# Kernel optimization log

Measured on AMD Instinct MI355X. Metric: run time of the kernel, lower is better.

The kernel has to match this reference:

```python
import jax, jax.numpy as jnp
import numpy as np

ALPHA = 0.2          # LeakyReLU negative slope
NEG = -9e15          # mask fill value, as in pyGAT GraphAttentionLayer
N, NIN, NHID, NOUT = 4096, 64, 32, 64
NHEADS, D_INT = 8, 32
H_INT = max(1, int(NHEADS * 0.25))   # 2 intent heads
H_SP = NHEADS - H_INT                # 6 spatial heads


def setup_inputs() -> dict:
    key = jax.random.key(0)
    ks = jax.random.split(key, 10)
    x = jax.random.normal(ks[0], (N, NIN), dtype=jnp.float32)
    adj = (jax.random.uniform(ks[1], (N, N)) < 0.01).astype(jnp.float32)
    adj = jnp.clip(adj + jnp.eye(N, dtype=jnp.float32), 0.0, 1.0)
    intent_embeds = jax.random.normal(ks[2], (N, D_INT), dtype=jnp.float32)
    # learned params (xavier-ish scale)
    def xav(k, shape):
        fan = shape[-2] if len(shape) > 1 else shape[-1]
        return jax.random.normal(k, shape, dtype=jnp.float32) / np.sqrt(fan)
    W_sp = xav(ks[3], (H_SP, NIN, NHID))       # spatial head projections
    a_sp = xav(ks[4], (H_SP, 2 * NHID))        # spatial attention vectors
    W_int = xav(ks[5], (H_INT, NIN, NHID))     # intent head projections
    a_int = xav(ks[6], (H_INT, 2 * D_INT))     # intent attention vectors (over intent embeds)
    W_out = xav(ks[7], (NHID * NHEADS, NOUT))  # output GAT layer
    a_out = xav(ks[8], (2 * NOUT,))
    return {"x": x, "adj": adj, "intent_embeds": intent_embeds,
            "W_sp": W_sp, "a_sp": a_sp, "W_int": W_int, "a_int": a_int,
            "W_out": W_out, "a_out": a_out}


def _masked_attend(e, mask, Wh):
    # e: [H,N,N] raw scores, mask: [1,N,N] bool, Wh: [H,N,F]
    att = jax.nn.softmax(jnp.where(mask, e, NEG), axis=-1)
    return jnp.einsum('hij,hjf->hif', att, Wh)


def reference(x, adj, intent_embeds, W_sp, a_sp, W_int, a_int, W_out, a_out):
    mask = (adj > 0)[None]                                   # [1,N,N]
    # ---- spatial heads (standard GAT, batched over heads) ----
    Wh_s = jnp.einsum('nf,hfo->hno', x, W_sp)                # [Hs,N,nhid]
    f1 = jnp.einsum('hno,ho->hn', Wh_s, a_sp[:, :NHID])
    f2 = jnp.einsum('hno,ho->hn', Wh_s, a_sp[:, NHID:])
    e_s = jax.nn.leaky_relu(f1[:, :, None] + f2[:, None, :], ALPHA)
    h_s = jax.nn.elu(_masked_attend(e_s, mask, Wh_s))        # concat=True -> elu
    # ---- intent heads: scores from intent embeddings, values from Wh ----
    Wh_i = jnp.einsum('nf,hfo->hno', x, W_int)               # [Hi,N,nhid]
    g1 = jnp.einsum('nd,hd->hn', intent_embeds, a_int[:, :D_INT])
    g2 = jnp.einsum('nd,hd->hn', intent_embeds, a_int[:, D_INT:])
    e_i = jax.nn.leaky_relu(g1[:, :, None] + g2[:, None, :], ALPHA)
    h_i = jax.nn.elu(_masked_attend(e_i, mask, Wh_i))        # [Hi,N,nhid]
    # ---- concat heads along feature dim: [N, nheads*nhid] ----
    h = jnp.concatenate([h_s, h_i], axis=0).transpose(1, 0, 2).reshape(N, -1)
    # ---- output attention layer (concat=False: no elu) ----
    Who = h @ W_out                                          # [N,nout]
    o1 = Who @ a_out[:NOUT]
    o2 = Who @ a_out[NOUT:]
    e_o = jax.nn.leaky_relu(o1[:, None] + o2[None, :], ALPHA)
    att_o = jax.nn.softmax(jnp.where(mask[0], e_o, NEG), axis=-1)
    out = att_o @ Who
    return jnp.tanh(out)
```

## Files before the change

### kernel.cpp

```cpp
#include <hip/hip_runtime.h>

#define N      4096
#define NIN    64
#define NHID   32
#define NOUT   64
#define NHEADS 8
#define H_SP   6
#define D_INT  32
#define MAXDEG 128
#define NPB    4
#define ALPHA  0.2f

__global__ __launch_bounds__(256) void k_fused1(
    const float* __restrict__ x, const float* __restrict__ ie,
    const float4* __restrict__ adj4,
    const float* __restrict__ Wsp, const float* __restrict__ asp,
    const float* __restrict__ Wint, const float* __restrict__ aint,
    float* __restrict__ Wh_t, float* __restrict__ src, float* __restrict__ dst_t,
    int* __restrict__ col, int* __restrict__ deg)
{
    const int nb   = blockIdx.x * NPB;
    const int tid  = threadIdx.x;
    const int wv   = tid >> 6, lane = tid & 63;
    const int h    = tid >> 5, f    = tid & 31;

    __shared__ float xs[NPB][NIN];
    __shared__ float ies[NPB][D_INT];

    xs[tid >> 6][tid & 63] = x[nb * NIN + tid];
    if (tid < NPB * D_INT) ies[tid >> 5][tid & 31] = ie[nb * D_INT + tid];
    __syncthreads();

    const float* W = (h < H_SP) ? (Wsp + h * NIN * NHID)
                                : (Wint + (h - H_SP) * NIN * NHID);
    float acc[NPB] = {0.f, 0.f, 0.f, 0.f};
#pragma unroll
    for (int c = 0; c < NIN; ++c) {
        const float wval = W[c * NHID + f];
#pragma unroll
        for (int m = 0; m < NPB; ++m) acc[m] += xs[m][c] * wval;
    }
#pragma unroll
    for (int m = 0; m < NPB; ++m)
        Wh_t[(size_t)(nb + m) * 256 + tid] = acc[m];

    const float a1v = (h < H_SP) ? asp[h * 64 + f]      : aint[(h - H_SP) * 64 + f];
    const float a2v = (h < H_SP) ? asp[h * 64 + 32 + f] : aint[(h - H_SP) * 64 + 32 + f];
#pragma unroll
    for (int m = 0; m < NPB; ++m) {
        const float b = (h < H_SP) ? acc[m] : ies[m][f];
        float s1 = b * a1v, s2 = b * a2v;
#pragma unroll
        for (int mm = 16; mm >= 1; mm >>= 1) {
            s1 += __shfl_xor(s1, mm);
            s2 += __shfl_xor(s2, mm);
        }
        if (f == 0) { src[h * N + nb + m] = s1; dst_t[(nb + m) * 8 + h] = s2; }
    }

    const int r = nb + wv;
    const float4* row = adj4 + (size_t)r * (N / 4);
    int cnt = 0;
#pragma unroll 4
    for (int t = 0; t < 16; ++t) {
        float4 v = row[t * 64 + lane];
        unsigned nib = (v.x > 0.f ? 1u : 0u) | (v.y > 0.f ? 2u : 0u)
                     | (v.z > 0.f ? 4u : 0u) | (v.w > 0.f ? 8u : 0u);
        int c = __popc(nib);
        int scan = c;
#pragma unroll
        for (int m = 1; m <= 32; m <<= 1) {
            int o = __shfl_up(scan, m);
            if (lane >= m) scan += o;
        }
        int pos = cnt + scan - c;
        int idx0 = (t * 64 + lane) * 4;
        if (nib) {
            if (nib & 1u) { if (pos < MAXDEG) col[r * MAXDEG + pos] = idx0;     ++pos; }
            if (nib & 2u) { if (pos < MAXDEG) col[r * MAXDEG + pos] = idx0 + 1; ++pos; }
            if (nib & 4u) { if (pos < MAXDEG) col[r * MAXDEG + pos] = idx0 + 2; ++pos; }
            if (nib & 8u) { if (pos < MAXDEG) col[r * MAXDEG + pos] = idx0 + 3; ++pos; }
        }
        cnt += __shfl(scan, 63);
    }
    if (lane == 0) deg[r] = (cnt < MAXDEG) ? cnt : MAXDEG;
}

__global__ __launch_bounds__(256) void k_attn1who(
    const int* __restrict__ col, const int* __restrict__ deg,
    const float* __restrict__ Wh_t, const float* __restrict__ src,
    const float* __restrict__ dst_t, const float* __restrict__ Wout,
    const float* __restrict__ aout,
    float* __restrict__ Who, float* __restrict__ o1, float* __restrict__ o2)
{
    const int r   = blockIdx.x;
    const int tid = threadIdx.x;
    const int h   = tid >> 5, lane = tid & 31;

    __shared__ int   cs[MAXDEG];
    __shared__ float w[NHEADS][MAXDEG];
    __shared__ float hs[NHEADS * NHID];
    __shared__ float part[4][NOUT];

    const int d  = deg[r];
    const int d8 = (d + 7) & ~7;
    for (int k = tid; k < MAXDEG; k += 256)
        cs[k] = (k < d) ? col[r * MAXDEG + k] : 0;
    __syncthreads();

    const float sr = src[h * N + r];
    float ev[4];
    float mx = -3.4e38f;
#pragma unroll
    for (int t = 0; t < 4; ++t) {
        int k = lane + t * 32;
        float e = -3.4e38f;
        if (k < d) {
            e = sr + dst_t[cs[k] * 8 + h];
            e = e > 0.f ? e : ALPHA * e;
        }
        ev[t] = e;
        mx = fmaxf(mx, e);
    }
#pragma unroll
    for (int m = 16; m >= 1; m >>= 1) mx = fmaxf(mx, __shfl_xor(mx, m));

    float sum = 0.f;
#pragma unroll
    for (int t = 0; t < 4; ++t) {
        int k = lane + t * 32;
        float p = (k < d) ? __expf(ev[t] - mx) : 0.f;
        ev[t] = p;
        sum += p;
    }
#pragma unroll
    for (int m = 16; m >= 1; m >>= 1) sum += __shfl_xor(sum, m);
    const float inv = 1.f / sum;

#pragma unroll
    for (int t = 0; t < 4; ++t) {
        int k = lane + t * 32;
        w[h][k] = (k < d) ? ev[t] * inv : 0.f;
    }
    __syncthreads();

    float acc0 = 0.f, acc1 = 0.f;
    for (int k = 0; k < d8; k += 8) {
        int4   ja = *(const int4*)  &cs[k];
        int4   jb = *(const int4*)  &cs[k + 4];
        float4 wa = *(const float4*)&w[h][k];
        float4 wb = *(const float4*)&w[h][k + 4];
        float g0 = Wh_t[(size_t)ja.x * 256 + tid];
        float g1 = Wh_t[(size_t)ja.y * 256 + tid];
        float g2 = Wh_t[(size_t)ja.z * 256 + tid];
        float g3 = Wh_t[(size_t)ja.w * 256 + tid];
        float g4 = Wh_t[(size_t)jb.x * 256 + tid];
        float g5 = Wh_t[(size_t)jb.y * 256 + tid];
        float g6 = Wh_t[(size_t)jb.z * 256 + tid];
        float g7 = Wh_t[(size_t)jb.w * 256 + tid];
        acc0 += wa.x * g0 + wa.y * g1 + wa.z * g2 + wa.w * g3;
        acc1 += wb.x * g4 + wb.y * g5 + wb.z * g6 + wb.w * g7;
    }
    float acc = acc0 + acc1;
    acc = acc > 0.f ? acc : __expf(acc) - 1.f;
    hs[tid] = acc;
    __syncthreads();

    const int fo = tid & 63, q = tid >> 6;
    float p = 0.f;
#pragma unroll
    for (int c = q * 64; c < q * 64 + 64; ++c) p += hs[c] * Wout[c * NOUT + fo];
    part[q][fo] = p;
    __syncthreads();

    if (tid < 64) {
        float who = part[0][tid] + part[1][tid] + part[2][tid] + part[3][tid];
        Who[(size_t)r * NOUT + tid] = who;
        float v1 = who * aout[tid];
        float v2 = who * aout[NOUT + tid];
#pragma unroll
        for (int m = 32; m >= 1; m >>= 1) {
            v1 += __shfl_xor(v1, m);
            v2 += __shfl_xor(v2, m);
        }
        if (tid == 0) { o1[r] = v1; o2[r] = v2; }
    }
}

__global__ __launch_bounds__(256) void k_attn2(
    const int* __restrict__ col, const int* __restrict__ deg,
    const float* __restrict__ Who, const float* __restrict__ o1,
    const float* __restrict__ o2, float* __restrict__ out)
{
    const int r   = blockIdx.x;
    const int tid = threadIdx.x;
    const int wv  = tid >> 6, lane = tid & 63;

    __shared__ int   cs[MAXDEG];
    __shared__ float w[MAXDEG];
    __shared__ float part[4][NOUT];
    __shared__ float redm[4], reds[4];

    const int d = deg[r];
    for (int k = tid; k < MAXDEG; k += 256)
        cs[k] = (k < d) ? col[r * MAXDEG + k] : 0;
    __syncthreads();

    const float sr = o1[r];
    float e = -3.4e38f;
    if (tid < d) {
        e = sr + o2[cs[tid]];
        e = e > 0.f ? e : ALPHA * e;
    }
    float mx = e;
#pragma unroll
    for (int m = 32; m >= 1; m >>= 1) mx = fmaxf(mx, __shfl_xor(mx, m));
    if (lane == 0) redm[wv] = mx;
    __syncthreads();
    mx = fmaxf(fmaxf(redm[0], redm[1]), fmaxf(redm[2], redm[3]));

    float p = (tid < d) ? __expf(e - mx) : 0.f;
    float s = p;
#pragma unroll
    for (int m = 32; m >= 1; m >>= 1) s += __shfl_xor(s, m);
    if (lane == 0) reds[wv] = s;
    __syncthreads();
    const float inv = 1.f / (reds[0] + reds[1] + reds[2] + reds[3]);
    if (tid < MAXDEG) w[tid] = p * inv;
    __syncthreads();

    const int kup = (d + 31) & ~31;
    float acc0 = 0.f, acc1 = 0.f;
    for (int k = wv * 8; k < kup; k += 32) {
        int4   ja = *(const int4*)  &cs[k];
        int4   jb = *(const int4*)  &cs[k + 4];
        float4 wa = *(const float4*)&w[k];
        float4 wb = *(const float4*)&w[k + 4];
        acc0 += wa.x * Who[(size_t)ja.x * NOUT + lane];
        acc0 += wa.y * Who[(size_t)ja.y * NOUT + lane];
        acc0 += wa.z * Who[(size_t)ja.z * NOUT + lane];
        acc0 += wa.w * Who[(size_t)ja.w * NOUT + lane];
        acc1 += wb.x * Who[(size_t)jb.x * NOUT + lane];
        acc1 += wb.y * Who[(size_t)jb.y * NOUT + lane];
        acc1 += wb.z * Who[(size_t)jb.z * NOUT + lane];
        acc1 += wb.w * Who[(size_t)jb.w * NOUT + lane];
    }
    part[wv][lane] = acc0 + acc1;
    __syncthreads();

    if (tid < NOUT)
        out[(size_t)r * NOUT + tid] =
            tanhf(part[0][tid] + part[1][tid] + part[2][tid] + part[3][tid]);
}

extern "C" void kernel_launch(void* const* d_in, const int* in_sizes, int n_in,
                              void* d_out, int out_size, void* d_ws, size_t ws_size,
                              hipStream_t stream) {
    const float* x    = (const float*)d_in[0];
    const float* adj  = (const float*)d_in[1];
    const float* ie   = (const float*)d_in[2];
    const float* Wsp  = (const float*)d_in[3];
    const float* asp  = (const float*)d_in[4];
    const float* Wint = (const float*)d_in[5];
    const float* aint = (const float*)d_in[6];
    const float* Wout = (const float*)d_in[7];
    const float* aout = (const float*)d_in[8];
    float* out = (float*)d_out;

    float* ws    = (float*)d_ws;
    float* Wh_t  = ws;
    float* src   = Wh_t + 1048576;
    float* dst_t = src  + 32768;
    float* Who   = dst_t + 32768;
    float* o1    = Who  + 262144;
    float* o2    = o1   + 4096;
    int*   col   = (int*)(o2 + 4096);
    int*   deg   = col + 4096 * MAXDEG;

    k_fused1  <<<N / NPB, 256, 0, stream>>>(x, ie, (const float4*)adj, Wsp, asp,
                                            Wint, aint, Wh_t, src, dst_t, col, deg);
    k_attn1who<<<N,       256, 0, stream>>>(col, deg, Wh_t, src, dst_t, Wout, aout,
                                            Who, o1, o2);
    k_attn2   <<<N,       256, 0, stream>>>(col, deg, Who, o1, o2, out);
}
```

Before: 154.7 us.

## Use ballot compaction, batch rows per block, and wave-per-row output attention

The adjacency compaction replaces shuffle-based prefix scans with per-component ballots and mbcnt to compute write positions. The first attention kernel now handles two rows per block, so each Wout load is shared and launch overhead drops. The output attention kernel maps one wavefront per row and broadcasts neighbor indices and weights with readlane, removing shared memory and block barriers. The x tile is also transposed so the projection reads four rows with one vector LDS load. Gather loops for two rows run to the larger degree, which may waste some work.

```diff
diff --git a/kernel.cpp b/kernel.cpp
--- a/kernel.cpp
+++ b/kernel.cpp
@@ -9,7 +9,13 @@
 #define D_INT  32
 #define MAXDEG 128
 #define NPB    4
+#define NPB2   2
 #define ALPHA  0.2f
+
+__device__ __forceinline__ int mbcnt64(unsigned long long m) {
+    return __builtin_amdgcn_mbcnt_hi((unsigned)(m >> 32),
+           __builtin_amdgcn_mbcnt_lo((unsigned)m, 0u));
+}
 
 __global__ __launch_bounds__(256) void k_fused1(
     const float* __restrict__ x, const float* __restrict__ ie,
@@ -24,10 +30,10 @@
     const int wv   = tid >> 6, lane = tid & 63;
     const int h    = tid >> 5, f    = tid & 31;
 
-    __shared__ float xs[NPB][NIN];
+    __shared__ float xs_t[NIN][NPB];
     __shared__ float ies[NPB][D_INT];
 
-    xs[tid >> 6][tid & 63] = x[nb * NIN + tid];
+    xs_t[tid & 63][tid >> 6] = x[nb * NIN + tid];
     if (tid < NPB * D_INT) ies[tid >> 5][tid & 31] = ie[nb * D_INT + tid];
     __syncthreads();
 
@@ -37,8 +43,9 @@
 #pragma unroll
     for (int c = 0; c < NIN; ++c) {
         const float wval = W[c * NHID + f];
-#pragma unroll
-        for (int m = 0; m < NPB; ++m) acc[m] += xs[m][c] * wval;
+        const float4 xv  = *(const float4*)&xs_t[c][0];
+        acc[0] += xv.x * wval; acc[1] += xv.y * wval;
+        acc[2] += xv.z * wval; acc[3] += xv.w * wval;
     }
 #pragma unroll
     for (int m = 0; m < NPB; ++m)
@@ -64,24 +71,22 @@
 #pragma unroll 4
     for (int t = 0; t < 16; ++t) {
         float4 v = row[t * 64 + lane];
-        unsigned nib = (v.x > 0.f ? 1u : 0u) | (v.y > 0.f ? 2u : 0u)
-                     | (v.z > 0.f ? 4u : 0u) | (v.w > 0.f ? 8u : 0u);
-        int c = __popc(nib);
-        int scan = c;
-#pragma unroll
-        for (int m = 1; m <= 32; m <<= 1) {
-            int o = __shfl_up(scan, m);
-            if (lane >= m) scan += o;
-        }
-        int pos = cnt + scan - c;
-        int idx0 = (t * 64 + lane) * 4;
-        if (nib) {
-            if (nib & 1u) { if (pos < MAXDEG) col[r * MAXDEG + pos] = idx0;     ++pos; }
-            if (nib & 2u) { if (pos < MAXDEG) col[r * MAXDEG + pos] = idx0 + 1; ++pos; }
-            if (nib & 4u) { if (pos < MAXDEG) col[r * MAXDEG + pos] = idx0 + 2; ++pos; }
-            if (nib & 8u) { if (pos < MAXDEG) col[r * MAXDEG + pos] = idx0 + 3; ++pos; }
-        }
-        cnt += __shfl(scan, 63);
+        unsigned long long bx = __ballot(v.x > 0.f);
+        unsigned long long by = __ballot(v.y > 0.f);
+        unsigned long long bz = __ballot(v.z > 0.f);
+        unsigned long long bw = __ballot(v.w > 0.f);
+        const int tx = __popcll(bx), ty = __popcll(by);
+        const int tz = __popcll(bz), tw = __popcll(bw);
+        const int idx0 = (t * 64 + lane) * 4;
+        const int px = cnt + mbcnt64(bx);
+        const int py = cnt + tx + mbcnt64(by);
+        const int pz = cnt + tx + ty + mbcnt64(bz);
+        const int pw = cnt + tx + ty + tz + mbcnt64(bw);
+        if (v.x > 0.f && px < MAXDEG) col[r * MAXDEG + px] = idx0;
+        if (v.y > 0.f && py < MAXDEG) col[r * MAXDEG + py] = idx0 + 1;
+        if (v.z > 0.f && pz < MAXDEG) col[r * MAXDEG + pz] = idx0 + 2;
+        if (v.w > 0.f && pw < MAXDEG) col[r * MAXDEG + pw] = idx0 + 3;
+        cnt += tx + ty + tz + tw;
     }
     if (lane == 0) deg[r] = (cnt < MAXDEG) ? cnt : MAXDEG;
 }
@@ -93,97 +98,109 @@
     const float* __restrict__ aout,
     float* __restrict__ Who, float* __restrict__ o1, float* __restrict__ o2)
 {
-    const int r   = blockIdx.x;
+    const int r0  = blockIdx.x * NPB2;
     const int tid = threadIdx.x;
     const int h   = tid >> 5, lane = tid & 31;
 
-    __shared__ int   cs[MAXDEG];
-    __shared__ float w[NHEADS][MAXDEG];
-    __shared__ float hs[NHEADS * NHID];
-    __shared__ float part[4][NOUT];
-
-    const int d  = deg[r];
-    const int d8 = (d + 7) & ~7;
-    for (int k = tid; k < MAXDEG; k += 256)
-        cs[k] = (k < d) ? col[r * MAXDEG + k] : 0;
-    __syncthreads();
-
-    const float sr = src[h * N + r];
-    float ev[4];
-    float mx = -3.4e38f;
-#pragma unroll
-    for (int t = 0; t < 4; ++t) {
-        int k = lane + t * 32;
-        float e = -3.4e38f;
-        if (k < d) {
-            e = sr + dst_t[cs[k] * 8 + h];
-            e = e > 0.f ? e : ALPHA * e;
-        }
-        ev[t] = e;
-        mx = fmaxf(mx, e);
-    }
-#pragma unroll
-    for (int m = 16; m >= 1; m >>= 1) mx = fmaxf(mx, __shfl_xor(mx, m));
-
-    float sum = 0.f;
-#pragma unroll
-    for (int t = 0; t < 4; ++t) {
-        int k = lane + t * 32;
-        float p = (k < d) ? __expf(ev[t] - mx) : 0.f;
-        ev[t] = p;
-        sum += p;
-    }
-#pragma unroll
-    for (int m = 16; m >= 1; m >>= 1) sum += __shfl_xor(sum, m);
-    const float inv = 1.f / sum;
-
-#pragma unroll
-    for (int t = 0; t < 4; ++t) {
-        int k = lane + t * 32;
-        w[h][k] = (k < d) ? ev[t] * inv : 0.f;
-    }
-    __syncthreads();
-
-    float acc0 = 0.f, acc1 = 0.f;
-    for (int k = 0; k < d8; k += 8) {
-        int4   ja = *(const int4*)  &cs[k];
-        int4   jb = *(const int4*)  &cs[k + 4];
-        float4 wa = *(const float4*)&w[h][k];
-        float4 wb = *(const float4*)&w[h][k + 4];
-        float g0 = Wh_t[(size_t)ja.x * 256 + tid];
-        float g1 = Wh_t[(size_t)ja.y * 256 + tid];
-        float g2 = Wh_t[(size_t)ja.z * 256 + tid];
-        float g3 = Wh_t[(size_t)ja.w * 256 + tid];
-        float g4 = Wh_t[(size_t)jb.x * 256 + tid];
-        float g5 = Wh_t[(size_t)jb.y * 256 + tid];
-        float g6 = Wh_t[(size_t)jb.z * 256 + tid];
-        float g7 = Wh_t[(size_t)jb.w * 256 + tid];
-        acc0 += wa.x * g0 + wa.y * g1 + wa.z * g2 + wa.w * g3;
-        acc1 += wb.x * g4 + wb.y * g5 + wb.z * g6 + wb.w * g7;
-    }
-    float acc = acc0 + acc1;
-    acc = acc > 0.f ? acc : __expf(acc) - 1.f;
-    hs[tid] = acc;
+    __shared__ int   cs[NPB2][MAXDEG];
+    __shared__ float w[NPB2][NHEADS][MAXDEG];
+    __shared__ float hs[NPB2][NHEADS * NHID];
+    __shared__ float part[NPB2][4][NOUT];
+
+    const int d0 = deg[r0], d1 = deg[r0 + 1];
+    {
+        const int m = tid >> 7, k = tid & 127;
+        const int dm = m ? d1 : d0;
+        cs[m][k] = (k < dm) ? col[(r0 + m) * MAXDEG + k] : 0;
+    }
+    __syncthreads();
+
+#pragma unroll
+    for (int m = 0; m < NPB2; ++m) {
+        const int dm = m ? d1 : d0;
+        const float sr = src[h * N + r0 + m];
+        float ev[4];
+        float mx = -3.4e38f;
+#pragma unroll
+        for (int t = 0; t < 4; ++t) {
+            const int k = lane + t * 32;
+            float e = -3.4e38f;
+            if (k < dm) {
+                e = sr + dst_t[cs[m][k] * 8 + h];
+                e = e > 0.f ? e : ALPHA * e;
+            }
+            ev[t] = e;
+            mx = fmaxf(mx, e);
+        }
+#pragma unroll
+        for (int mm = 16; mm >= 1; mm >>= 1) mx = fmaxf(mx, __shfl_xor(mx, mm));
+        float sum = 0.f;
+#pragma unroll
+        for (int t = 0; t < 4; ++t) {
+            const int k = lane + t * 32;
+            float p = (k < dm) ? __expf(ev[t] - mx) : 0.f;
+            ev[t] = p;
+            sum += p;
+        }
+#pragma unroll
+        for (int mm = 16; mm >= 1; mm >>= 1) sum += __shfl_xor(sum, mm);
+        const float inv = 1.f / sum;
+#pragma unroll
+        for (int t = 0; t < 4; ++t) w[m][h][lane + t * 32] = ev[t] * inv;
+    }
+    __syncthreads();
+
+    const int d8a = (d0 + 7) & ~7, d8b = (d1 + 7) & ~7;
+    const int d8m = d8a > d8b ? d8a : d8b;
+    float a0 = 0.f, a1 = 0.f, c0 = 0.f, c1 = 0.f;
+    for (int k = 0; k < d8m; k += 8) {
+        int4   ja = *(const int4*)  &cs[0][k];
+        int4   jA = *(const int4*)  &cs[0][k + 4];
+        int4   jb = *(const int4*)  &cs[1][k];
+        int4   jB = *(const int4*)  &cs[1][k + 4];
+        float4 wa = *(const float4*)&w[0][h][k];
+        float4 wA = *(const float4*)&w[0][h][k + 4];
+        float4 wb = *(const float4*)&w[1][h][k];
+        float4 wB = *(const float4*)&w[1][h][k + 4];
+        a0 += wa.x * Wh_t[(size_t)ja.x * 256 + tid] + wa.y * Wh_t[(size_t)ja.y * 256 + tid]
+            + wa.z * Wh_t[(size_t)ja.z * 256 + tid] + wa.w * Wh_t[(size_t)ja.w * 256 + tid];
+        a1 += wA.x * Wh_t[(size_t)jA.x * 256 + tid] + wA.y * Wh_t[(size_t)jA.y * 256 + tid]
+            + wA.z * Wh_t[(size_t)jA.z * 256 + tid] + wA.w * Wh_t[(size_t)jA.w * 256 + tid];
+        c0 += wb.x * Wh_t[(size_t)jb.x * 256 + tid] + wb.y * Wh_t[(size_t)jb.y * 256 + tid]
+            + wb.z * Wh_t[(size_t)jb.z * 256 + tid] + wb.w * Wh_t[(size_t)jb.w * 256 + tid];
+        c1 += wB.x * Wh_t[(size_t)jB.x * 256 + tid] + wB.y * Wh_t[(size_t)jB.y * 256 + tid]
+            + wB.z * Wh_t[(size_t)jB.z * 256 + tid] + wB.w * Wh_t[(size_t)jB.w * 256 + tid];
+    }
+    float av = a0 + a1; av = av > 0.f ? av : __expf(av) - 1.f;
+    float cv = c0 + c1; cv = cv > 0.f ? cv : __expf(cv) - 1.f;
+    hs[0][tid] = av;
+    hs[1][tid] = cv;
     __syncthreads();
 
     const int fo = tid & 63, q = tid >> 6;
-    float p = 0.f;
-#pragma unroll
-    for (int c = q * 64; c < q * 64 + 64; ++c) p += hs[c] * Wout[c * NOUT + fo];
-    part[q][fo] = p;
-    __syncthreads();
-
-    if (tid < 64) {
-        float who = part[0][tid] + part[1][tid] + part[2][tid] + part[3][tid];
-        Who[(size_t)r * NOUT + tid] = who;
-        float v1 = who * aout[tid];
-        float v2 = who * aout[NOUT + tid];
-#pragma unroll
-        for (int m = 32; m >= 1; m >>= 1) {
-            v1 += __shfl_xor(v1, m);
-            v2 += __shfl_xor(v2, m);
-        }
-        if (tid == 0) { o1[r] = v1; o2[r] = v2; }
+    float p0 = 0.f, p1 = 0.f;
+#pragma unroll
+    for (int c = q * 64; c < q * 64 + 64; ++c) {
+        const float wv_ = Wout[c * NOUT + fo];
+        p0 += hs[0][c] * wv_;
+        p1 += hs[1][c] * wv_;
+    }
+    part[0][q][fo] = p0;
+    part[1][q][fo] = p1;
+    __syncthreads();
+
+    if (tid < 128) {
+        const int m = tid >> 6, fo2 = tid & 63;
+        float who = part[m][0][fo2] + part[m][1][fo2] + part[m][2][fo2] + part[m][3][fo2];
+        Who[(size_t)(r0 + m) * NOUT + fo2] = who;
+        float v1 = who * aout[fo2];
+        float v2 = who * aout[NOUT + fo2];
+#pragma unroll
+        for (int mm = 32; mm >= 1; mm >>= 1) {
+            v1 += __shfl_xor(v1, mm);
+            v2 += __shfl_xor(v2, mm);
+        }
+        if (fo2 == 0) { o1[r0 + m] = v1; o2[r0 + m] = v2; }
     }
 }
 
@@ -192,65 +209,46 @@
     const float* __restrict__ Who, const float* __restrict__ o1,
     const float* __restrict__ o2, float* __restrict__ out)
 {
-    const int r   = blockIdx.x;
-    const int tid = threadIdx.x;
-    const int wv  = tid >> 6, lane = tid & 63;
-
-    __shared__ int   cs[MAXDEG];
-    __shared__ float w[MAXDEG];
-    __shared__ float part[4][NOUT];
-    __shared__ float redm[4], reds[4];
-
-    const int d = deg[r];
-    for (int k = tid; k < MAXDEG; k += 256)
-        cs[k] = (k < d) ? col[r * MAXDEG + k] : 0;
-    __syncthreads();
-
+    const int tid  = threadIdx.x;
+    const int wv   = tid >> 6, lane = tid & 63;
+    const int r    = blockIdx.x * 4 + wv;
+
+    const int d  = deg[r];
+    const int j0 = (lane < d)      ? col[r * MAXDEG + lane]      : 0;
+    const int j1 = (lane + 64 < d) ? col[r * MAXDEG + 64 + lane] : 0;
     const float sr = o1[r];
-    float e = -3.4e38f;
-    if (tid < d) {
-        e = sr + o2[cs[tid]];
-        e = e > 0.f ? e : ALPHA * e;
-    }
-    float mx = e;
+
+    float e0 = -3.4e38f, e1 = -3.4e38f;
+    if (lane < d)      { float e = sr + o2[j0]; e0 = e > 0.f ? e : ALPHA * e; }
+    if (lane + 64 < d) { float e = sr + o2[j1]; e1 = e > 0.f ? e : ALPHA * e; }
+    float mx = fmaxf(e0, e1);
 #pragma unroll
     for (int m = 32; m >= 1; m >>= 1) mx = fmaxf(mx, __shfl_xor(mx, m));
-    if (lane == 0) redm[wv] = mx;
-    __syncthreads();
-    mx = fmaxf(fmaxf(redm[0], redm[1]), fmaxf(redm[2], redm[3]));
-
-    float p = (tid < d) ? __expf(e - mx) : 0.f;
-    float s = p;
+    float p0 = (lane < d)      ? __expf(e0 - mx) : 0.f;
+    float p1 = (lane + 64 < d) ? __expf(e1 - mx) : 0.f;
+    float s = p0 + p1;
 #pragma unroll
     for (int m = 32; m >= 1; m >>= 1) s += __shfl_xor(s, m);
-    if (lane == 0) reds[wv] = s;
-    __syncthreads();
-    const float inv = 1.f / (reds[0] + reds[1] + reds[2] + reds[3]);
-    if (tid < MAXDEG) w[tid] = p * inv;
-    __syncthreads();
-
-    const int kup = (d + 31) & ~31;
-    float acc0 = 0.f, acc1 = 0.f;
-    for (int k = wv * 8; k < kup; k += 32) {
-        int4   ja = *(const int4*)  &cs[k];
-        int4   jb = *(const int4*)  &cs[k + 4];
-        float4 wa = *(const float4*)&w[k];
-        float4 wb = *(const float4*)&w[k + 4];
-        acc0 += wa.x * Who[(size_t)ja.x * NOUT + lane];
-        acc0 += wa.y * Who[(size_t)ja.y * NOUT + lane];
-        acc0 += wa.z * Who[(size_t)ja.z * NOUT + lane];
-        acc0 += wa.w * Who[(size_t)ja.w * NOUT + lane];
-        acc1 += wb.x * Who[(size_t)jb.x * NOUT + lane];
-        acc1 += wb.y * Who[(size_t)jb.y * NOUT + lane];
-        acc1 += wb.z * Who[(size_t)jb.z * NOUT + lane];
-        acc1 += wb.w * Who[(size_t)jb.w * NOUT + lane];
-    }
-    part[wv][lane] = acc0 + acc1;
-    __syncthreads();
-
-    if (tid < NOUT)
-        out[(size_t)r * NOUT + tid] =
-            tanhf(part[0][tid] + part[1][tid] + part[2][tid] + part[3][tid]);
+    const float inv = 1.f / s;
+    const float w0 = p0 * inv, w1 = p1 * inv;
+
+    float acc = 0.f;
+    const int dlo = d < 64 ? d : 64;
+#pragma unroll 4
+    for (int k = 0; k < dlo; ++k) {
+        const int   j  = __builtin_amdgcn_readlane(j0, k);
+        const float wt = __uint_as_float(
+            __builtin_amdgcn_readlane(__float_as_uint(w0), k));
+        acc += wt * Who[(size_t)j * NOUT + lane];
+    }
+#pragma unroll 2
+    for (int k = 64; k < d; ++k) {
+        const int   j  = __builtin_amdgcn_readlane(j1, k - 64);
+        const float wt = __uint_as_float(
+            __builtin_amdgcn_readlane(__float_as_uint(w1), k - 64));
+        acc += wt * Who[(size_t)j * NOUT + lane];
+    }
+    out[(size_t)r * NOUT + lane] = tanhf(acc);
 }
 
 extern "C" void kernel_launch(void* const* d_in, const int* in_sizes, int n_in,
@@ -277,9 +275,9 @@
     int*   col   = (int*)(o2 + 4096);
     int*   deg   = col + 4096 * MAXDEG;
 
-    k_fused1  <<<N / NPB, 256, 0, stream>>>(x, ie, (const float4*)adj, Wsp, asp,
-                                            Wint, aint, Wh_t, src, dst_t, col, deg);
-    k_attn1who<<<N,       256, 0, stream>>>(col, deg, Wh_t, src, dst_t, Wout, aout,
-                                            Who, o1, o2);
-    k_attn2   <<<N,       256, 0, stream>>>(col, deg, Who, o1, o2, out);
-}
+    k_fused1  <<<N / NPB,  256, 0, stream>>>(x, ie, (const float4*)adj, Wsp, asp,
+                                             Wint, aint, Wh_t, src, dst_t, col, deg);
+    k_attn1who<<<N / NPB2, 256, 0, stream>>>(col, deg, Wh_t, src, dst_t, Wout, aout,
+                                             Who, o1, o2);
+    k_attn2   <<<N / 4,    256, 0, stream>>>(col, deg, Who, o1, o2, out);
+}
```

After: 170.3 us. +10.1%, slower.
